# Kernel tuning notes

Hardware: AMD Instinct MI355X
Metric: run time of the kernel (lower is better)

Reference implementation:

```python
import jax, jax.numpy as jnp
import numpy as np
from jax import lax

B, S, E, H, V, C = 256, 128, 512, 1024, 128, 18


def setup_inputs() -> dict:
    key = jax.random.key(0)
    ks = jax.random.split(key, 12)
    x_in = jax.random.randint(ks[0], (B, S), 0, V, dtype=jnp.int64)
    x_lengths = jax.random.randint(ks[1], (B,), 1, S + 1, dtype=jnp.int64)
    emb = jax.random.normal(ks[2], (V, E), dtype=jnp.float32) * 0.05
    emb = emb.at[0].set(0.0)  # padding_idx=0
    W_ih = jax.random.normal(ks[3], (H, E), dtype=jnp.float32) * (1.0 / np.sqrt(H))
    b_ih = jax.random.normal(ks[4], (H,), dtype=jnp.float32) * 0.01
    W_hh = jax.random.normal(ks[5], (H, H), dtype=jnp.float32) * (1.0 / np.sqrt(H))
    b_hh = jax.random.normal(ks[6], (H,), dtype=jnp.float32) * 0.01
    W1 = jax.random.normal(ks[7], (H, H), dtype=jnp.float32) * (1.0 / np.sqrt(H))
    b1 = jax.random.normal(ks[8], (H,), dtype=jnp.float32) * 0.01
    W2 = jax.random.normal(ks[9], (C, H), dtype=jnp.float32) * (1.0 / np.sqrt(H))
    b2 = jax.random.normal(ks[10], (C,), dtype=jnp.float32) * 0.01
    return {"x_in": x_in, "x_lengths": x_lengths, "emb": emb,
            "W_ih": W_ih, "b_ih": b_ih, "W_hh": W_hh, "b_hh": b_hh,
            "W1": W1, "b1": b1, "W2": W2, "b2": b2}


def reference(x_in, x_lengths, emb, W_ih, b_ih, W_hh, b_hh, W1, b1, W2, b2):
    # Embedding lookup: [B, S, E]
    x = emb[x_in]
    # Precompute the input-to-hidden projection for all timesteps: [S, B, H]
    pre = jnp.einsum('bse,he->sbh', x, W_ih) + b_ih

    def step(h, p_t):
        h_new = jnp.tanh(p_t + h @ W_hh.T + b_hh)
        return h_new, h_new

    h0 = jnp.zeros((x.shape[0], W_hh.shape[0]), dtype=x.dtype)
    _, hiddens = lax.scan(step, h0, pre)          # [S, B, H]
    hiddens = jnp.transpose(hiddens, (1, 0, 2))   # [B, S, H]

    # column_gather: final hidden state per sequence length
    idx = (x_lengths - 1).astype(jnp.int32)
    last = hiddens[jnp.arange(hiddens.shape[0]), idx]  # [B, H]

    # MLP head (dropout treated as identity / eval mode)
    y = jax.nn.relu(last @ W1.T + b1)
    return y @ W2.T + b2
```

## Files before the change

kernel.cpp:

```cpp
#include <hip/hip_runtime.h>
#include <hip/hip_bf16.h>

#define BB 256
#define SS 128
#define EE 512
#define HH 1024
#define VV 128
#define CC 18

typedef _Float16 f16x8 __attribute__((ext_vector_type(8)));
typedef _Float16 f16x4 __attribute__((ext_vector_type(4)));
typedef float    f32x4 __attribute__((ext_vector_type(4)));

#define HBUF_OFF  0x000000
#define FLAGS_OFF 0x200000
#define EP_OFF    0x210000
#define LAST_OFF  0x290000
#define Z_OFF     0x390000

__device__ inline f16x8 cvt8(f32x4 a, f32x4 b) {
  f16x8 r;
  r[0] = (_Float16)a.x; r[1] = (_Float16)a.y; r[2] = (_Float16)a.z; r[3] = (_Float16)a.w;
  r[4] = (_Float16)b.x; r[5] = (_Float16)b.y; r[6] = (_Float16)b.z; r[7] = (_Float16)b.w;
  return r;
}

__device__ inline f16x8 ld_cp16(const _Float16* p) {
  const unsigned long long* q = (const unsigned long long*)p;
  union { unsigned long long u[2]; f16x8 v; } r;
  r.u[0] = __hip_atomic_load(q + 0, __ATOMIC_RELAXED, __HIP_MEMORY_SCOPE_AGENT);
  r.u[1] = __hip_atomic_load(q + 1, __ATOMIC_RELAXED, __HIP_MEMORY_SCOPE_AGENT);
  return r.v;
}
__device__ inline void st_cp8(_Float16* p, f16x4 v) {
  union { f16x4 v; unsigned long long u; } c; c.v = v;
  __hip_atomic_store((unsigned long long*)p, c.u, __ATOMIC_RELAXED,
                     __HIP_MEMORY_SCOPE_AGENT);
}

__device__ inline void group_wait(const int* gflags, int lane, int target) {
  while (true) {
    int f = __hip_atomic_load(&gflags[lane & 15], __ATOMIC_RELAXED,
                              __HIP_MEMORY_SCOPE_AGENT);
    if (__all(f >= target)) break;
    __builtin_amdgcn_s_sleep(1);
  }
  asm volatile("" ::: "memory");
}

__device__ inline float tanh_fast(float x) {
  const float e = __expf(-2.0f * fabsf(x));
  return copysignf((1.0f - e) / (1.0f + e), x);
}

__global__ __launch_bounds__(256) void k_embproj(const float* __restrict__ emb,
                                                 const float* __restrict__ W_ih,
                                                 const float* __restrict__ b_ih,
                                                 const float* __restrict__ b_hh,
                                                 float* __restrict__ ep) {
  __shared__ float red[4][16][66];
  const int bid = blockIdx.x;
  const int v0 = (bid & 7) * 16;
  const int h0 = (bid >> 3) * 64;
  const int tid = threadIdx.x;
  const int w = tid >> 6, lane = tid & 63, lr = lane & 15, lk = lane >> 4;

  f32x4 acc[4] = {};
  const int vrow = v0 + lr;
#pragma unroll
  for (int ki = 0; ki < 4; ++ki) {
    const int k = w * 128 + ki * 32 + lk * 8;
    const f32x4* pa = (const f32x4*)(emb + vrow * EE + k);
    f16x8 af = cvt8(pa[0], pa[1]);
#pragma unroll
    for (int nt = 0; nt < 4; ++nt) {
      const int hcol = h0 + nt * 16 + lr;
      const f32x4* pb = (const f32x4*)(W_ih + hcol * EE + k);
      f16x8 bf = cvt8(pb[0], pb[1]);
      acc[nt] = __builtin_amdgcn_mfma_f32_16x16x32_f16(af, bf, acc[nt], 0, 0, 0);
    }
  }
#pragma unroll
  for (int nt = 0; nt < 4; ++nt)
#pragma unroll
    for (int j = 0; j < 4; ++j)
      red[w][lk * 4 + j][nt * 16 + lr] = acc[nt][j];
  __syncthreads();

  const int r = tid >> 4, cg = tid & 15, cc0 = cg * 4;
  const int vvr = v0 + r;
#pragma unroll
  for (int i = 0; i < 4; ++i) {
    const int hcol = h0 + cc0 + i;
    float s = red[0][r][cc0 + i] + red[1][r][cc0 + i] +
              red[2][r][cc0 + i] + red[3][r][cc0 + i];
    ep[vvr * HH + hcol] = s + b_ih[hcol] + b_hh[hcol];
  }
}

__global__ __launch_bounds__(256, 1) void k_rnn(const float* __restrict__ W_hh,
                                                const int* __restrict__ x_in,
                                                const int* __restrict__ x_len,
                                                const float* __restrict__ ep,
                                                _Float16* __restrict__ hbuf,
                                                int* __restrict__ flags,
                                                float* __restrict__ lastb) {
  __shared__ float red[4][16][68];
  __shared__ int xin[16][128];
  __shared__ int len1[16];

  const int bid = blockIdx.x;
  const int g = bid & 15;
  const int c = bid >> 4;
  const int row0 = g * 16, col0 = c * 64;
  const int tid = threadIdx.x;
  const int w = tid >> 6, lane = tid & 63, lr = lane & 15, lk = lane >> 4;
  int* gflags = flags + g * 16;

  for (int i = tid; i < 16 * SS; i += 256) {
    const int r_ = i >> 7, s_ = i & 127;
    xin[r_][s_] = x_in[(row0 + r_) * SS + s_];
  }
  if (tid < 16) len1[tid] = x_len[row0 + tid] - 1;

  f16x8 wreg[4][8];
#pragma unroll
  for (int nt = 0; nt < 4; ++nt) {
    const int col = col0 + nt * 16 + lr;
#pragma unroll
    for (int ki = 0; ki < 8; ++ki) {
      const int k = w * 256 + ki * 32 + lk * 8;
      const f32x4* pw = (const f32x4*)(W_hh + col * HH + k);
      wreg[nt][ki] = cvt8(pw[0], pw[1]);
    }
  }
  __syncthreads();

  int gmax = 0;
#pragma unroll
  for (int r16 = 0; r16 < 16; ++r16) gmax = max(gmax, len1[r16]);

  const int arow = row0 + lr;
  const int r = tid >> 4, cc0 = (tid & 15) * 4;
  const int grow = row0 + r;

  {
    const int vv = xin[r][0];
    const f32x4 pre4 = *(const f32x4*)(ep + vv * HH + col0 + cc0);
    float th[4];
    th[0] = tanh_fast(pre4.x); th[1] = tanh_fast(pre4.y);
    th[2] = tanh_fast(pre4.z); th[3] = tanh_fast(pre4.w);

    if (len1[r] == 0) {
      f32x4 o; o.x = th[0]; o.y = th[1]; o.z = th[2]; o.w = th[3];
      *(f32x4*)(lastb + (size_t)grow * HH + col0 + cc0) = o;
    }
    if (gmax >= 1) {
      f16x4 h4, l4;
#pragma unroll
      for (int i = 0; i < 4; ++i) {
        const _Float16 hh = (_Float16)th[i];
        h4[i] = hh;
        l4[i] = (_Float16)((th[i] - (float)hh) * 4096.0f);
      }
      st_cp8(hbuf + ((size_t)(1 * 2 + 0) * BB + grow) * HH + col0 + cc0, h4);
      st_cp8(hbuf + ((size_t)(1 * 2 + 1) * BB + grow) * HH + col0 + cc0, l4);
      __syncthreads();
      if (tid == 0)
        __hip_atomic_store(&gflags[c], 1, __ATOMIC_RELAXED, __HIP_MEMORY_SCOPE_AGENT);
      group_wait(gflags, lane, 1);
    }
  }

  for (int t = 1; t <= gmax; ++t) {
    const int bufR = t & 1;
    const _Float16* hr_hi = hbuf + ((size_t)(bufR * 2 + 0) * BB + arow) * HH;
    const _Float16* hr_lo = hbuf + ((size_t)(bufR * 2 + 1) * BB + arow) * HH;

    const int vv = xin[r][t];
    const f32x4 pre4 = *(const f32x4*)(ep + vv * HH + col0 + cc0);

    f16x8 ahi[8], alo[8];
#pragma unroll
    for (int ki = 0; ki < 8; ++ki) {
      const int k = w * 256 + ki * 32 + lk * 8;
      ahi[ki] = ld_cp16(hr_hi + k);
      alo[ki] = ld_cp16(hr_lo + k);
    }

    f32x4 acch[4] = {};
    f32x4 accl[4] = {};
#pragma unroll
    for (int ki = 0; ki < 8; ++ki) {
#pragma unroll
      for (int nt = 0; nt < 4; ++nt) {
        acch[nt] = __builtin_amdgcn_mfma_f32_16x16x32_f16(ahi[ki], wreg[nt][ki], acch[nt], 0, 0, 0);
        accl[nt] = __builtin_amdgcn_mfma_f32_16x16x32_f16(alo[ki], wreg[nt][ki], accl[nt], 0, 0, 0);
      }
    }
#pragma unroll
    for (int nt = 0; nt < 4; ++nt)
#pragma unroll
      for (int j = 0; j < 4; ++j)
        red[w][lk * 4 + j][nt * 16 + lr] = acch[nt][j] + accl[nt][j] * (1.0f / 4096.0f);
    __syncthreads();

    const f32x4 s0 = *(const f32x4*)&red[0][r][cc0];
    const f32x4 s1 = *(const f32x4*)&red[1][r][cc0];
    const f32x4 s2 = *(const f32x4*)&red[2][r][cc0];
    const f32x4 s3 = *(const f32x4*)&red[3][r][cc0];
    const f32x4 sv = (s0 + s1) + (s2 + s3);

    float th[4];
    th[0] = tanh_fast(sv.x + pre4.x);
    th[1] = tanh_fast(sv.y + pre4.y);
    th[2] = tanh_fast(sv.z + pre4.z);
    th[3] = tanh_fast(sv.w + pre4.w);

    if (len1[r] == t) {
      f32x4 o; o.x = th[0]; o.y = th[1]; o.z = th[2]; o.w = th[3];
      *(f32x4*)(lastb + (size_t)grow * HH + col0 + cc0) = o;
    }

    if (t < gmax) {
      const int bufW = bufR ^ 1;
      f16x4 h4, l4;
#pragma unroll
      for (int i = 0; i < 4; ++i) {
        const _Float16 hh = (_Float16)th[i];
        h4[i] = hh;
        l4[i] = (_Float16)((th[i] - (float)hh) * 4096.0f);
      }
      st_cp8(hbuf + ((size_t)(bufW * 2 + 0) * BB + grow) * HH + col0 + cc0, h4);
      st_cp8(hbuf + ((size_t)(bufW * 2 + 1) * BB + grow) * HH + col0 + cc0, l4);

      __syncthreads();
      if (tid == 0)
        __hip_atomic_store(&gflags[c], t + 1, __ATOMIC_RELAXED, __HIP_MEMORY_SCOPE_AGENT);
      group_wait(gflags, lane, t + 1);
    }
  }
}

__global__ __launch_bounds__(256) void k_mlp1(const float* __restrict__ lastb,
                                              const float* __restrict__ W1,
                                              const float* __restrict__ b1,
                                              float* __restrict__ z) {
  __shared__ float red[4][16][66];
  const int bid = blockIdx.x;
  const int row0 = (bid & 15) * 16, col0 = (bid >> 4) * 64;
  const int tid = threadIdx.x;
  const int w = tid >> 6, lane = tid & 63, lr = lane & 15, lk = lane >> 4;
  const int arow = row0 + lr;

  f32x4 acch[4] = {};
  f32x4 accl[4] = {};
#pragma unroll
  for (int ki = 0; ki < 8; ++ki) {
    const int k = w * 256 + ki * 32 + lk * 8;
    const f32x4* pa = (const f32x4*)(lastb + (size_t)arow * HH + k);
    f32x4 a0 = pa[0], a1 = pa[1];
    f16x8 ahi, alo;
#pragma unroll
    for (int i = 0; i < 4; ++i) {
      float v0 = (i == 0) ? a0.x : (i == 1) ? a0.y : (i == 2) ? a0.z : a0.w;
      float v1 = (i == 0) ? a1.x : (i == 1) ? a1.y : (i == 2) ? a1.z : a1.w;
      _Float16 h0 = (_Float16)v0, h1 = (_Float16)v1;
      ahi[i] = h0; ahi[i + 4] = h1;
      alo[i] = (_Float16)((v0 - (float)h0) * 4096.0f);
      alo[i + 4] = (_Float16)((v1 - (float)h1) * 4096.0f);
    }
#pragma unroll
    for (int nt = 0; nt < 4; ++nt) {
      const int colw = col0 + nt * 16 + lr;
      const f32x4* pb = (const f32x4*)(W1 + (size_t)colw * HH + k);
      f16x8 bf = cvt8(pb[0], pb[1]);
      acch[nt] = __builtin_amdgcn_mfma_f32_16x16x32_f16(ahi, bf, acch[nt], 0, 0, 0);
      accl[nt] = __builtin_amdgcn_mfma_f32_16x16x32_f16(alo, bf, accl[nt], 0, 0, 0);
    }
  }
#pragma unroll
  for (int nt = 0; nt < 4; ++nt)
#pragma unroll
    for (int j = 0; j < 4; ++j)
      red[w][lk * 4 + j][nt * 16 + lr] = acch[nt][j] + accl[nt][j] * (1.0f / 4096.0f);
  __syncthreads();

  const int r = tid >> 4, cc0 = (tid & 15) * 4;
  const int grow = row0 + r;
#pragma unroll
  for (int i = 0; i < 4; ++i) {
    const int col = col0 + cc0 + i;
    float s = red[0][r][cc0 + i] + red[1][r][cc0 + i] +
              red[2][r][cc0 + i] + red[3][r][cc0 + i] + b1[col];
    z[(size_t)grow * HH + col] = fmaxf(s, 0.0f);
  }
}

__global__ __launch_bounds__(256) void k_mlp2(const float* __restrict__ z,
                                              const float* __restrict__ W2,
                                              const float* __restrict__ b2,
                                              float* __restrict__ out) {
  __shared__ float redy[4][CC];
  const int b = blockIdx.x;
  const int tid = threadIdx.x;
  const int w = tid >> 6, lane = tid & 63;
  const int k = w * 256 + lane * 4;

  const f32x4 z4 = *(const f32x4*)(z + (size_t)b * HH + k);
  float part[CC];
#pragma unroll
  for (int c = 0; c < CC; ++c) {
    const f32x4 w4 = *(const f32x4*)(W2 + (size_t)c * HH + k);
    part[c] = z4.x * w4.x + z4.y * w4.y + z4.z * w4.z + z4.w * w4.w;
  }
#pragma unroll
  for (int c = 0; c < CC; ++c) {
    float v = part[c];
    for (int off = 32; off; off >>= 1) v += __shfl_down(v, off, 64);
    if (lane == 0) redy[w][c] = v;
  }
  __syncthreads();
  if (tid < CC)
    out[b * CC + tid] = redy[0][tid] + redy[1][tid] + redy[2][tid] + redy[3][tid] + b2[tid];
}

extern "C" void kernel_launch(void* const* d_in, const int* in_sizes, int n_in,
                              void* d_out, int out_size, void* d_ws, size_t ws_size,
                              hipStream_t stream) {
  const int*   x_in  = (const int*)d_in[0];
  const int*   x_len = (const int*)d_in[1];
  const float* emb   = (const float*)d_in[2];
  const float* W_ih  = (const float*)d_in[3];
  const float* b_ih  = (const float*)d_in[4];
  const float* W_hh  = (const float*)d_in[5];
  const float* b_hh  = (const float*)d_in[6];
  const float* W1    = (const float*)d_in[7];
  const float* b1    = (const float*)d_in[8];
  const float* W2    = (const float*)d_in[9];
  const float* b2    = (const float*)d_in[10];

  char* ws = (char*)d_ws;
  _Float16* hbuf = (_Float16*)(ws + HBUF_OFF);
  int* flags     = (int*)(ws + FLAGS_OFF);
  float* ep      = (float*)(ws + EP_OFF);
  float* lastb   = (float*)(ws + LAST_OFF);
  float* z       = (float*)(ws + Z_OFF);

  (void)hipMemsetAsync(flags, 0, 16 * 16 * 4, stream);

  hipLaunchKernelGGL(k_embproj, dim3(128), dim3(256), 0, stream, emb, W_ih, b_ih, b_hh, ep);
  hipLaunchKernelGGL(k_rnn,    dim3(256), dim3(256), 0, stream, W_hh, x_in, x_len, ep, hbuf, flags, lastb);
  hipLaunchKernelGGL(k_mlp1,   dim3(256), dim3(256), 0, stream, lastb, W1, b1, z);
  hipLaunchKernelGGL(k_mlp2,   dim3(256), dim3(256), 0, stream, z, W2, b2, (float*)d_out);
}
```

Before: 803.4 us.

## Replace per-step flag barrier with data-embedded step tags in hidden-state buffer

Drops the separate per-group flag array, along with the block barrier and flag store after each step. The low two mantissa bits of every fourth fp16 hi/lo value now carry a step tag, and consumers spin until the tags they loaded match the current step. The reduction scratch is double-buffered so the trailing block barrier can go. This removes a serialising barrier and flag round trip from the critical path of each step, at the cost of slightly perturbing the hidden values, retry loops on the loads, and a larger memset of the buffer.

New measurement: 849.3 us. 1.06x slower.

```diff
diff --git a/kernel.cpp b/kernel.cpp
--- a/kernel.cpp
+++ b/kernel.cpp
@@ -13,7 +13,6 @@
 typedef float    f32x4 __attribute__((ext_vector_type(4)));
 
 #define HBUF_OFF  0x000000
-#define FLAGS_OFF 0x200000
 #define EP_OFF    0x210000
 #define LAST_OFF  0x290000
 #define Z_OFF     0x390000
@@ -32,20 +31,29 @@
   r.u[1] = __hip_atomic_load(q + 1, __ATOMIC_RELAXED, __HIP_MEMORY_SCOPE_AGENT);
   return r.v;
 }
-__device__ inline void st_cp8(_Float16* p, f16x4 v) {
-  union { f16x4 v; unsigned long long u; } c; c.v = v;
-  __hip_atomic_store((unsigned long long*)p, c.u, __ATOMIC_RELAXED,
-                     __HIP_MEMORY_SCOPE_AGENT);
-}
-
-__device__ inline void group_wait(const int* gflags, int lane, int target) {
-  while (true) {
-    int f = __hip_atomic_load(&gflags[lane & 15], __ATOMIC_RELAXED,
-                              __HIP_MEMORY_SCOPE_AGENT);
-    if (__all(f >= target)) break;
-    __builtin_amdgcn_s_sleep(1);
-  }
-  asm volatile("" ::: "memory");
+
+__device__ inline void pack_store(_Float16* dhi, _Float16* dlo, const float th[4], int tg) {
+  union { unsigned short us[4]; unsigned long long u; } H, L;
+#pragma unroll
+  for (int i = 0; i < 4; ++i) {
+    union { _Float16 f; unsigned short b; } hc; hc.f = (_Float16)th[i];
+    unsigned short hb = hc.b;
+    if (i == 3) hb = (unsigned short)((hb & 0xFFFCu) | (unsigned)tg);
+    H.us[i] = hb;
+    union { unsigned short b; _Float16 f; } hd; hd.b = hb;
+    const float lv = (th[i] - (float)hd.f) * 4096.0f;
+    union { _Float16 f; unsigned short b; } lc; lc.f = (_Float16)lv;
+    unsigned short lb = lc.b;
+    if (i == 3) lb = (unsigned short)((lb & 0xFFFCu) | (unsigned)tg);
+    L.us[i] = lb;
+  }
+  __hip_atomic_store((unsigned long long*)dhi, H.u, __ATOMIC_RELAXED, __HIP_MEMORY_SCOPE_AGENT);
+  __hip_atomic_store((unsigned long long*)dlo, L.u, __ATOMIC_RELAXED, __HIP_MEMORY_SCOPE_AGENT);
+}
+
+__device__ inline int tag_bad(f16x8 v, unsigned tg) {
+  union { f16x8 f; unsigned u[4]; } c; c.f = v;
+  return (int)((((c.u[1] >> 16) ^ tg) | ((c.u[3] >> 16) ^ tg)) & 3u);
 }
 
 __device__ inline float tanh_fast(float x) {
@@ -103,9 +111,8 @@
                                                 const int* __restrict__ x_len,
                                                 const float* __restrict__ ep,
                                                 _Float16* __restrict__ hbuf,
-                                                int* __restrict__ flags,
                                                 float* __restrict__ lastb) {
-  __shared__ float red[4][16][68];
+  __shared__ float red[2][4][16][68];
   __shared__ int xin[16][128];
   __shared__ int len1[16];
 
@@ -115,7 +122,6 @@
   const int row0 = g * 16, col0 = c * 64;
   const int tid = threadIdx.x;
   const int w = tid >> 6, lane = tid & 63, lr = lane & 15, lk = lane >> 4;
-  int* gflags = flags + g * 16;
 
   for (int i = tid; i < 16 * SS; i += 256) {
     const int r_ = i >> 7, s_ = i & 127;
@@ -155,37 +161,45 @@
       f32x4 o; o.x = th[0]; o.y = th[1]; o.z = th[2]; o.w = th[3];
       *(f32x4*)(lastb + (size_t)grow * HH + col0 + cc0) = o;
     }
-    if (gmax >= 1) {
-      f16x4 h4, l4;
-#pragma unroll
-      for (int i = 0; i < 4; ++i) {
-        const _Float16 hh = (_Float16)th[i];
-        h4[i] = hh;
-        l4[i] = (_Float16)((th[i] - (float)hh) * 4096.0f);
-      }
-      st_cp8(hbuf + ((size_t)(1 * 2 + 0) * BB + grow) * HH + col0 + cc0, h4);
-      st_cp8(hbuf + ((size_t)(1 * 2 + 1) * BB + grow) * HH + col0 + cc0, l4);
-      __syncthreads();
-      if (tid == 0)
-        __hip_atomic_store(&gflags[c], 1, __ATOMIC_RELAXED, __HIP_MEMORY_SCOPE_AGENT);
-      group_wait(gflags, lane, 1);
-    }
+    if (gmax >= 1)
+      pack_store(hbuf + ((size_t)(1 * 2 + 0) * BB + grow) * HH + col0 + cc0,
+                 hbuf + ((size_t)(1 * 2 + 1) * BB + grow) * HH + col0 + cc0, th, 1);
   }
 
   for (int t = 1; t <= gmax; ++t) {
     const int bufR = t & 1;
+    const unsigned tg = (unsigned)(t & 3);
     const _Float16* hr_hi = hbuf + ((size_t)(bufR * 2 + 0) * BB + arow) * HH;
     const _Float16* hr_lo = hbuf + ((size_t)(bufR * 2 + 1) * BB + arow) * HH;
 
     const int vv = xin[r][t];
     const f32x4 pre4 = *(const f32x4*)(ep + vv * HH + col0 + cc0);
 
+    {
+      const _Float16* sp = hbuf + ((size_t)(bufR * 2 + 0) * BB + row0 + (lane & 15)) * HH
+                           + (w * 4 + (lane >> 4)) * 64;
+      for (;;) {
+        unsigned long long s = __hip_atomic_load((const unsigned long long*)sp,
+                                 __ATOMIC_RELAXED, __HIP_MEMORY_SCOPE_AGENT);
+        if (__all((((int)(s >> 48)) & 3) == (int)tg)) break;
+        __builtin_amdgcn_s_sleep(1);
+      }
+    }
+
     f16x8 ahi[8], alo[8];
-#pragma unroll
-    for (int ki = 0; ki < 8; ++ki) {
-      const int k = w * 256 + ki * 32 + lk * 8;
-      ahi[ki] = ld_cp16(hr_hi + k);
-      alo[ki] = ld_cp16(hr_lo + k);
+    for (;;) {
+#pragma unroll
+      for (int ki = 0; ki < 8; ++ki) {
+        const int k = w * 256 + ki * 32 + lk * 8;
+        ahi[ki] = ld_cp16(hr_hi + k);
+        alo[ki] = ld_cp16(hr_lo + k);
+      }
+      int bad = 0;
+#pragma unroll
+      for (int ki = 0; ki < 8; ++ki)
+        bad |= tag_bad(ahi[ki], tg) | tag_bad(alo[ki], tg);
+      if (!__any(bad)) break;
+      __builtin_amdgcn_s_sleep(1);
     }
 
     f32x4 acch[4] = {};
@@ -198,17 +212,18 @@
         accl[nt] = __builtin_amdgcn_mfma_f32_16x16x32_f16(alo[ki], wreg[nt][ki], accl[nt], 0, 0, 0);
       }
     }
+    const int p = t & 1;
 #pragma unroll
     for (int nt = 0; nt < 4; ++nt)
 #pragma unroll
       for (int j = 0; j < 4; ++j)
-        red[w][lk * 4 + j][nt * 16 + lr] = acch[nt][j] + accl[nt][j] * (1.0f / 4096.0f);
+        red[p][w][lk * 4 + j][nt * 16 + lr] = acch[nt][j] + accl[nt][j] * (1.0f / 4096.0f);
     __syncthreads();
 
-    const f32x4 s0 = *(const f32x4*)&red[0][r][cc0];
-    const f32x4 s1 = *(const f32x4*)&red[1][r][cc0];
-    const f32x4 s2 = *(const f32x4*)&red[2][r][cc0];
-    const f32x4 s3 = *(const f32x4*)&red[3][r][cc0];
+    const f32x4 s0 = *(const f32x4*)&red[p][0][r][cc0];
+    const f32x4 s1 = *(const f32x4*)&red[p][1][r][cc0];
+    const f32x4 s2 = *(const f32x4*)&red[p][2][r][cc0];
+    const f32x4 s3 = *(const f32x4*)&red[p][3][r][cc0];
     const f32x4 sv = (s0 + s1) + (s2 + s3);
 
     float th[4];
@@ -224,20 +239,9 @@
 
     if (t < gmax) {
       const int bufW = bufR ^ 1;
-      f16x4 h4, l4;
-#pragma unroll
-      for (int i = 0; i < 4; ++i) {
-        const _Float16 hh = (_Float16)th[i];
-        h4[i] = hh;
-        l4[i] = (_Float16)((th[i] - (float)hh) * 4096.0f);
-      }
-      st_cp8(hbuf + ((size_t)(bufW * 2 + 0) * BB + grow) * HH + col0 + cc0, h4);
-      st_cp8(hbuf + ((size_t)(bufW * 2 + 1) * BB + grow) * HH + col0 + cc0, l4);
-
-      __syncthreads();
-      if (tid == 0)
-        __hip_atomic_store(&gflags[c], t + 1, __ATOMIC_RELAXED, __HIP_MEMORY_SCOPE_AGENT);
-      group_wait(gflags, lane, t + 1);
+      pack_store(hbuf + ((size_t)(bufW * 2 + 0) * BB + grow) * HH + col0 + cc0,
+                 hbuf + ((size_t)(bufW * 2 + 1) * BB + grow) * HH + col0 + cc0,
+                 th, (int)((t + 1) & 3));
     }
   }
 }
@@ -342,15 +346,14 @@
 
   char* ws = (char*)d_ws;
   _Float16* hbuf = (_Float16*)(ws + HBUF_OFF);
-  int* flags     = (int*)(ws + FLAGS_OFF);
   float* ep      = (float*)(ws + EP_OFF);
   float* lastb   = (float*)(ws + LAST_OFF);
   float* z       = (float*)(ws + Z_OFF);
 
-  (void)hipMemsetAsync(flags, 0, 16 * 16 * 4, stream);
+  (void)hipMemsetAsync(hbuf, 0, 0x200000, stream);
 
   hipLaunchKernelGGL(k_embproj, dim3(128), dim3(256), 0, stream, emb, W_ih, b_ih, b_hh, ep);
-  hipLaunchKernelGGL(k_rnn,    dim3(256), dim3(256), 0, stream, W_hh, x_in, x_len, ep, hbuf, flags, lastb);
+  hipLaunchKernelGGL(k_rnn,    dim3(256), dim3(256), 0, stream, W_hh, x_in, x_len, ep, hbuf, lastb);
   hipLaunchKernelGGL(k_mlp1,   dim3(256), dim3(256), 0, stream, lastb, W1, b1, z);
   hipLaunchKernelGGL(k_mlp2,   dim3(256), dim3(256), 0, stream, z, W2, b2, (float*)d_out);
 }
```

## Stage W_hh in LDS and replace per-block flag polling with per-step counters

Applied to the files above, without the earlier changes.

The recurrent kernel now keeps its 64-column slice of W_hh as padded fp16 in shared memory instead of 32 vector registers per lane. This frees registers but adds LDS reads inside the MFMA loop. The group barrier also changes: instead of every lane polling 16 per-block flags, one thread atomically increments a per-timestep counter and spins until it reaches 16, then the block syncs. This cuts polling traffic at the cost of an extra __syncthreads per step.

New measurement: 765.6 us. 1.05x faster.

```diff
diff --git a/kernel.cpp b/kernel.cpp
--- a/kernel.cpp
+++ b/kernel.cpp
@@ -18,6 +18,8 @@
 #define LAST_OFF  0x290000
 #define Z_OFF     0x390000
 
+#define WPAD 1032
+
 __device__ inline f16x8 cvt8(f32x4 a, f32x4 b) {
   f16x8 r;
   r[0] = (_Float16)a.x; r[1] = (_Float16)a.y; r[2] = (_Float16)a.z; r[3] = (_Float16)a.w;
@@ -36,16 +38,6 @@
   union { f16x4 v; unsigned long long u; } c; c.v = v;
   __hip_atomic_store((unsigned long long*)p, c.u, __ATOMIC_RELAXED,
                      __HIP_MEMORY_SCOPE_AGENT);
-}
-
-__device__ inline void group_wait(const int* gflags, int lane, int target) {
-  while (true) {
-    int f = __hip_atomic_load(&gflags[lane & 15], __ATOMIC_RELAXED,
-                              __HIP_MEMORY_SCOPE_AGENT);
-    if (__all(f >= target)) break;
-    __builtin_amdgcn_s_sleep(1);
-  }
-  asm volatile("" ::: "memory");
 }
 
 __device__ inline float tanh_fast(float x) {
@@ -105,6 +97,7 @@
                                                 _Float16* __restrict__ hbuf,
                                                 int* __restrict__ flags,
                                                 float* __restrict__ lastb) {
+  __shared__ _Float16 wlds[64 * WPAD];
   __shared__ float red[4][16][68];
   __shared__ int xin[16][128];
   __shared__ int len1[16];
@@ -115,25 +108,22 @@
   const int row0 = g * 16, col0 = c * 64;
   const int tid = threadIdx.x;
   const int w = tid >> 6, lane = tid & 63, lr = lane & 15, lk = lane >> 4;
-  int* gflags = flags + g * 16;
-
+  int* gflags = flags + g * SS;
+
+  for (int idx = tid; idx < 64 * 256; idx += 256) {
+    const int col = idx >> 8;
+    const int kq  = (idx & 255) * 4;
+    const f32x4 v = *(const f32x4*)(W_hh + (size_t)(col0 + col) * HH + kq);
+    f16x4 hv;
+    hv[0] = (_Float16)v.x; hv[1] = (_Float16)v.y;
+    hv[2] = (_Float16)v.z; hv[3] = (_Float16)v.w;
+    *(f16x4*)(&wlds[col * WPAD + kq]) = hv;
+  }
   for (int i = tid; i < 16 * SS; i += 256) {
     const int r_ = i >> 7, s_ = i & 127;
     xin[r_][s_] = x_in[(row0 + r_) * SS + s_];
   }
   if (tid < 16) len1[tid] = x_len[row0 + tid] - 1;
-
-  f16x8 wreg[4][8];
-#pragma unroll
-  for (int nt = 0; nt < 4; ++nt) {
-    const int col = col0 + nt * 16 + lr;
-#pragma unroll
-    for (int ki = 0; ki < 8; ++ki) {
-      const int k = w * 256 + ki * 32 + lk * 8;
-      const f32x4* pw = (const f32x4*)(W_hh + col * HH + k);
-      wreg[nt][ki] = cvt8(pw[0], pw[1]);
-    }
-  }
   __syncthreads();
 
   int gmax = 0;
@@ -143,6 +133,7 @@
   const int arow = row0 + lr;
   const int r = tid >> 4, cc0 = (tid & 15) * 4;
   const int grow = row0 + r;
+  const int wbase = lr * WPAD + w * 256 + lk * 8;
 
   {
     const int vv = xin[r][0];
@@ -166,9 +157,15 @@
       st_cp8(hbuf + ((size_t)(1 * 2 + 0) * BB + grow) * HH + col0 + cc0, h4);
       st_cp8(hbuf + ((size_t)(1 * 2 + 1) * BB + grow) * HH + col0 + cc0, l4);
       __syncthreads();
-      if (tid == 0)
-        __hip_atomic_store(&gflags[c], 1, __ATOMIC_RELAXED, __HIP_MEMORY_SCOPE_AGENT);
-      group_wait(gflags, lane, 1);
+      if (tid == 0) {
+        __hip_atomic_fetch_add(&gflags[0], 1, __ATOMIC_RELAXED, __HIP_MEMORY_SCOPE_AGENT);
+        while (__hip_atomic_load(&gflags[0], __ATOMIC_RELAXED,
+                                 __HIP_MEMORY_SCOPE_AGENT) < 16) {
+          __builtin_amdgcn_s_sleep(1);
+        }
+      }
+      __syncthreads();
+      asm volatile("" ::: "memory");
     }
   }
 
@@ -194,8 +191,9 @@
     for (int ki = 0; ki < 8; ++ki) {
 #pragma unroll
       for (int nt = 0; nt < 4; ++nt) {
-        acch[nt] = __builtin_amdgcn_mfma_f32_16x16x32_f16(ahi[ki], wreg[nt][ki], acch[nt], 0, 0, 0);
-        accl[nt] = __builtin_amdgcn_mfma_f32_16x16x32_f16(alo[ki], wreg[nt][ki], accl[nt], 0, 0, 0);
+        const f16x8 wf = *(const f16x8*)(&wlds[wbase + nt * (16 * WPAD) + ki * 32]);
+        acch[nt] = __builtin_amdgcn_mfma_f32_16x16x32_f16(ahi[ki], wf, acch[nt], 0, 0, 0);
+        accl[nt] = __builtin_amdgcn_mfma_f32_16x16x32_f16(alo[ki], wf, accl[nt], 0, 0, 0);
       }
     }
 #pragma unroll
@@ -235,9 +233,15 @@
       st_cp8(hbuf + ((size_t)(bufW * 2 + 1) * BB + grow) * HH + col0 + cc0, l4);
 
       __syncthreads();
-      if (tid == 0)
-        __hip_atomic_store(&gflags[c], t + 1, __ATOMIC_RELAXED, __HIP_MEMORY_SCOPE_AGENT);
-      group_wait(gflags, lane, t + 1);
+      if (tid == 0) {
+        __hip_atomic_fetch_add(&gflags[t], 1, __ATOMIC_RELAXED, __HIP_MEMORY_SCOPE_AGENT);
+        while (__hip_atomic_load(&gflags[t], __ATOMIC_RELAXED,
+                                 __HIP_MEMORY_SCOPE_AGENT) < 16) {
+          __builtin_amdgcn_s_sleep(1);
+        }
+      }
+      __syncthreads();
+      asm volatile("" ::: "memory");
     }
   }
 }
@@ -347,7 +351,7 @@
   float* lastb   = (float*)(ws + LAST_OFF);
   float* z       = (float*)(ws + Z_OFF);
 
-  (void)hipMemsetAsync(flags, 0, 16 * 16 * 4, stream);
+  (void)hipMemsetAsync(flags, 0, 16 * SS * 4, stream);
 
   hipLaunchKernelGGL(k_embproj, dim3(128), dim3(256), 0, stream, emb, W_ih, b_ih, b_hh, ep);
   hipLaunchKernelGGL(k_rnn,    dim3(256), dim3(256), 0, stream, W_hh, x_in, x_len, ep, hbuf, flags, lastb);
```
